# Kernel optimization log

Hardware: AMD Instinct MI355X
Metric: run time of the kernel (lower is better)

## Reference

```python
import jax, jax.numpy as jnp
import numpy as np

NS, NT, D, H = 256, 16384, 3, 64
EPS = 1e-8  # smoothing_radius


def setup_inputs() -> dict:
    key = jax.random.key(0)
    ks = jax.random.split(key, 8)
    return {
        "reference_length": jnp.float32(1.0),
        "source_points": jax.random.normal(ks[0], (NS, D), jnp.float32),
        "target_points": jax.random.normal(ks[1], (NT, D), jnp.float32),
        "source_strengths": jax.random.normal(ks[2], (NS,), jnp.float32),
        "W1": jax.random.normal(ks[3], (1, H), jnp.float32),
        "b1": jnp.zeros((H,), jnp.float32),
        "pade_a": jax.random.normal(ks[4], (H, 3), jnp.float32) * 0.5,
        "pade_b": jax.random.normal(ks[5], (H, 2), jnp.float32) * 0.5,
        "W2": jax.random.normal(ks[6], (H, 2), jnp.float32) / jnp.sqrt(jnp.float32(H)),
        "b2": jnp.zeros((2,), jnp.float32),
    }


def reference(reference_length, source_points, target_points, source_strengths,
              W1, b1, pade_a, pade_b, W2, b2):
    # Pairwise relative positions: [T, S, D]
    r = target_points[:, None, :] - source_points[None, :, :]
    # Smoothed distance (smoothing_radius regularizes near r=0): [T, S]
    d = jnp.sqrt(jnp.sum(r * r, axis=-1) + EPS * EPS)
    # Dimensionless invariant feature: smoothed log-magnitude of r.
    # (With no source/global vectors, n_vectors_in=1 -> no SH pair features.)
    feat = jnp.log(d / reference_length)[..., None]            # [T, S, 1]
    # Pade rational network: linear -> per-channel rational activation -> linear
    x = feat @ W1 + b1                                          # [T, S, H]
    num = pade_a[:, 0] + pade_a[:, 1] * x + pade_a[:, 2] * x * x
    den = 1.0 + jnp.abs(pade_b[:, 0] * x + pade_b[:, 1] * x * x)
    h = num / den                                               # [T, S, H]
    out = h @ W2 + b2                                           # [T, S, 2]
    # Scatter (sum over sources) weighted by source strengths.
    scalar = jnp.einsum('ts,s->t', out[..., 0], source_strengths)      # [T]
    # Vector field: radial reprojection coefficient * unit r, summed over sources.
    r_hat = r / d[..., None]                                    # [T, S, D]
    vector = jnp.einsum('ts,tsd,s->td', out[..., 1], r_hat, source_strengths)
    # Pack scalar field 'phi' and vector field 'v' into one [T, 1+D] array.
    return jnp.concatenate([scalar[:, None], vector], axis=-1)
```

## Files before the change

### kernel.cpp

```cpp
#include <hip/hip_runtime.h>

#define NSRC 256
#define NTGT 16384
#define NH   64
#define TAB_N 4096
constexpr float TAB_LO = -10.0f;
constexpr float TAB_HI =  4.0f;
constexpr float TAB_STEP     = (TAB_HI - TAB_LO) / (float)TAB_N;
constexpr float TAB_INV_STEP = (float)TAB_N / (TAB_HI - TAB_LO);
constexpr float EPS2 = 1e-8f * 1e-8f;
constexpr float LN2  = 0.6931471805599453f;
constexpr int   TPB    = 256;
constexpr int   SCHUNK = 32;

__global__ __launch_bounds__(256)
void build_table(const float* __restrict__ W1, const float* __restrict__ b1,
                 const float* __restrict__ pa, const float* __restrict__ pb,
                 const float* __restrict__ W2, float2* __restrict__ tab)
{
    const int i = blockIdx.x * 256 + threadIdx.x;
    if (i > TAB_N) return;
    const float feat = TAB_LO + (float)i * TAB_STEP;
    float g0 = 0.f, g1 = 0.f;
    for (int h = 0; h < NH; ++h) {
        const float x   = fmaf(feat, W1[h], b1[h]);
        const float x2  = x * x;
        const float num = fmaf(x2, pa[h * 3 + 2], fmaf(x, pa[h * 3 + 1], pa[h * 3 + 0]));
        const float den = 1.0f + fabsf(fmaf(x2, pb[h * 2 + 1], x * pb[h * 2 + 0]));
        const float g   = num / den;
        g0 = fmaf(g, W2[h * 2 + 0], g0);
        g1 = fmaf(g, W2[h * 2 + 1], g1);
    }
    tab[i] = make_float2(g0, g1);
}

__global__ __launch_bounds__(TPB)
void field_kernel(const float* __restrict__ refL,
                  const float* __restrict__ src,
                  const float* __restrict__ tgt,
                  const float* __restrict__ str,
                  const float* __restrict__ b2,
                  const float2* __restrict__ gtab,
                  float* __restrict__ out)
{
    __shared__ float2 tab[TAB_N + 1];
    for (int j = threadIdx.x; j <= TAB_N; j += TPB) tab[j] = gtab[j];
    __syncthreads();

    const int t  = blockIdx.x * TPB + threadIdx.x;
    const int s0 = blockIdx.y * SCHUNK;
    const float tx = tgt[t * 3 + 0];
    const float ty = tgt[t * 3 + 1];
    const float tz = tgt[t * 3 + 2];
    const float logL = __builtin_amdgcn_logf(refL[0]) * LN2;
    const float K1 = 0.5f * LN2 * TAB_INV_STEP;
    const float K2 = (-logL - TAB_LO) * TAB_INV_STEP;
    const float b20 = b2[0], b21 = b2[1];

    float acc0 = 0.f, ax = 0.f, ay = 0.f, az = 0.f;
    #pragma unroll
    for (int i = 0; i < SCHUNK; ++i) {
        const int s = s0 + i;
        const float rx = tx - src[s * 3 + 0];
        const float ry = ty - src[s * 3 + 1];
        const float rz = tz - src[s * 3 + 2];
        const float d2 = fmaf(rx, rx, fmaf(ry, ry, fmaf(rz, rz, EPS2)));
        const float idxf = fmaf(__builtin_amdgcn_logf(d2), K1, K2);
        int ii = (int)floorf(idxf);
        ii = min(max(ii, 0), TAB_N - 1);
        const float frac = idxf - (float)ii;
        const float2 e0 = tab[ii];
        const float2 e1 = tab[ii + 1];
        const float g0 = fmaf(frac, e1.x - e0.x, e0.x);
        const float g1 = fmaf(frac, e1.y - e0.y, e0.y);
        const float invd = __builtin_amdgcn_rsqf(d2);
        const float w = str[s];
        acc0 = fmaf(g0 + b20, w, acc0);
        const float c = (g1 + b21) * w * invd;
        ax = fmaf(c, rx, ax);
        ay = fmaf(c, ry, ay);
        az = fmaf(c, rz, az);
    }

    atomicAdd(&out[t * 4 + 0], acc0);
    atomicAdd(&out[t * 4 + 1], ax);
    atomicAdd(&out[t * 4 + 2], ay);
    atomicAdd(&out[t * 4 + 3], az);
}

extern "C" void kernel_launch(void* const* d_in, const int* in_sizes, int n_in,
                              void* d_out, int out_size, void* d_ws, size_t ws_size,
                              hipStream_t stream) {
    const float* refL = (const float*)d_in[0];
    const float* src  = (const float*)d_in[1];
    const float* tgt  = (const float*)d_in[2];
    const float* str  = (const float*)d_in[3];
    const float* W1   = (const float*)d_in[4];
    const float* b1   = (const float*)d_in[5];
    const float* pa   = (const float*)d_in[6];
    const float* pb   = (const float*)d_in[7];
    const float* W2   = (const float*)d_in[8];
    const float* b2   = (const float*)d_in[9];
    float*  out  = (float*)d_out;
    float2* gtab = (float2*)d_ws;

    hipMemsetAsync(out, 0, (size_t)out_size * sizeof(float), stream);

    build_table<<<dim3((TAB_N + 256) / 256), dim3(256), 0, stream>>>(
        W1, b1, pa, pb, W2, gtab);

    dim3 grid(NTGT / TPB, NSRC / SCHUNK);
    field_kernel<<<grid, dim3(TPB), 0, stream>>>(
        refL, src, tgt, str, b2, gtab, out);
}
```

Measured before the change: 101.2 us.

## Reduce source groups in shared memory instead of atomics; pack table pairs

Each block now covers 64 targets, with four wavefronts each taking a quarter of the sources. Partial sums are combined in shared memory and written once, so the global atomics and the output memset go away. The lookup table is shrunk to 3072 entries and stored as float4 holding adjacent pairs, so interpolation needs a single LDS read. The table build also uses a fast reciprocal. In exchange, fewer blocks load the table and each runs a longer loop, and the coarser table adds interpolation error.

New measurement: 89.53 us. 1.13x faster.

```diff
diff --git a/kernel.cpp b/kernel.cpp
--- a/kernel.cpp
+++ b/kernel.cpp
@@ -3,7 +3,7 @@
 #define NSRC 256
 #define NTGT 16384
 #define NH   64
-#define TAB_N 4096
+#define TAB_N 3072
 constexpr float TAB_LO = -10.0f;
 constexpr float TAB_HI =  4.0f;
 constexpr float TAB_STEP     = (TAB_HI - TAB_LO) / (float)TAB_N;
@@ -11,7 +11,9 @@
 constexpr float EPS2 = 1e-8f * 1e-8f;
 constexpr float LN2  = 0.6931471805599453f;
 constexpr int   TPB    = 256;
-constexpr int   SCHUNK = 32;
+constexpr int   TGT_B  = 64;
+constexpr int   NGRP   = 4;
+constexpr int   SG     = NSRC / NGRP;
 
 __global__ __launch_bounds__(256)
 void build_table(const float* __restrict__ W1, const float* __restrict__ b1,
@@ -27,7 +29,7 @@
         const float x2  = x * x;
         const float num = fmaf(x2, pa[h * 3 + 2], fmaf(x, pa[h * 3 + 1], pa[h * 3 + 0]));
         const float den = 1.0f + fabsf(fmaf(x2, pb[h * 2 + 1], x * pb[h * 2 + 0]));
-        const float g   = num / den;
+        const float g   = num * __builtin_amdgcn_rcpf(den);
         g0 = fmaf(g, W2[h * 2 + 0], g0);
         g1 = fmaf(g, W2[h * 2 + 1], g1);
     }
@@ -43,12 +45,21 @@
                   const float2* __restrict__ gtab,
                   float* __restrict__ out)
 {
-    __shared__ float2 tab[TAB_N + 1];
-    for (int j = threadIdx.x; j <= TAB_N; j += TPB) tab[j] = gtab[j];
+    __shared__ float4 tab[TAB_N];
+    __shared__ float4 part[NGRP][TGT_B];
+
+    for (int j = threadIdx.x; j < TAB_N; j += TPB) {
+        const float2 a = gtab[j];
+        const float2 b = gtab[j + 1];
+        tab[j] = make_float4(a.x, a.y, b.x, b.y);
+    }
     __syncthreads();
 
-    const int t  = blockIdx.x * TPB + threadIdx.x;
-    const int s0 = blockIdx.y * SCHUNK;
+    const int jt = threadIdx.x & (TGT_B - 1);
+    const int g  = __builtin_amdgcn_readfirstlane(threadIdx.x >> 6);
+    const int t  = blockIdx.x * TGT_B + jt;
+    const int sb = g * SG;
+
     const float tx = tgt[t * 3 + 0];
     const float ty = tgt[t * 3 + 1];
     const float tz = tgt[t * 3 + 2];
@@ -58,9 +69,9 @@
     const float b20 = b2[0], b21 = b2[1];
 
     float acc0 = 0.f, ax = 0.f, ay = 0.f, az = 0.f;
-    #pragma unroll
-    for (int i = 0; i < SCHUNK; ++i) {
-        const int s = s0 + i;
+    #pragma unroll 16
+    for (int i = 0; i < SG; ++i) {
+        const int s = sb + i;
         const float rx = tx - src[s * 3 + 0];
         const float ry = ty - src[s * 3 + 1];
         const float rz = tz - src[s * 3 + 2];
@@ -69,10 +80,9 @@
         int ii = (int)floorf(idxf);
         ii = min(max(ii, 0), TAB_N - 1);
         const float frac = idxf - (float)ii;
-        const float2 e0 = tab[ii];
-        const float2 e1 = tab[ii + 1];
-        const float g0 = fmaf(frac, e1.x - e0.x, e0.x);
-        const float g1 = fmaf(frac, e1.y - e0.y, e0.y);
+        const float4 e = tab[ii];
+        const float g0 = fmaf(frac, e.z - e.x, e.x);
+        const float g1 = fmaf(frac, e.w - e.y, e.y);
         const float invd = __builtin_amdgcn_rsqf(d2);
         const float w = str[s];
         acc0 = fmaf(g0 + b20, w, acc0);
@@ -82,10 +92,21 @@
         az = fmaf(c, rz, az);
     }
 
-    atomicAdd(&out[t * 4 + 0], acc0);
-    atomicAdd(&out[t * 4 + 1], ax);
-    atomicAdd(&out[t * 4 + 2], ay);
-    atomicAdd(&out[t * 4 + 3], az);
+    part[g][jt] = make_float4(acc0, ax, ay, az);
+    __syncthreads();
+
+    if (threadIdx.x < TGT_B) {
+        const float4 p0 = part[0][jt];
+        const float4 p1 = part[1][jt];
+        const float4 p2 = part[2][jt];
+        const float4 p3 = part[3][jt];
+        float4 r;
+        r.x = (p0.x + p1.x) + (p2.x + p3.x);
+        r.y = (p0.y + p1.y) + (p2.y + p3.y);
+        r.z = (p0.z + p1.z) + (p2.z + p3.z);
+        r.w = (p0.w + p1.w) + (p2.w + p3.w);
+        ((float4*)out)[t] = r;
+    }
 }
 
 extern "C" void kernel_launch(void* const* d_in, const int* in_sizes, int n_in,
@@ -104,12 +125,9 @@
     float*  out  = (float*)d_out;
     float2* gtab = (float2*)d_ws;
 
-    hipMemsetAsync(out, 0, (size_t)out_size * sizeof(float), stream);
-
     build_table<<<dim3((TAB_N + 256) / 256), dim3(256), 0, stream>>>(
         W1, b1, pa, pb, W2, gtab);
 
-    dim3 grid(NTGT / TPB, NSRC / SCHUNK);
-    field_kernel<<<grid, dim3(TPB), 0, stream>>>(
+    field_kernel<<<dim3(NTGT / TGT_B), dim3(TPB), 0, stream>>>(
         refL, src, tgt, str, b2, gtab, out);
 }
```
